# Performance work log

Hardware: AMD Instinct MI355X
Metric: run time of the kernel (lower is better)

The kernel has to match this reference:

```python
import jax, jax.numpy as jnp
import numpy as np
import math

B, L, D, H = 8, 2048, 1024, 1024


def setup_inputs() -> dict:
    key = jax.random.key(0)
    ks = jax.random.split(key, 6)
    scale = 1.0 / math.sqrt(D)
    return {
        "input_q": jax.random.normal(ks[0], (B, L, D), dtype=jnp.float32),
        "input_k": jax.random.normal(ks[1], (B, L, D), dtype=jnp.float32),
        "k_mask": jax.random.uniform(ks[2], (B, L), dtype=jnp.float32),
        "Wq": jax.random.normal(ks[3], (D, H), dtype=jnp.float32) * scale,
        "bq": jnp.zeros((H,), dtype=jnp.float32),
        "Wk": jax.random.normal(ks[4], (D, H), dtype=jnp.float32) * scale,
        "bk": jnp.zeros((H,), dtype=jnp.float32),
    }


def reference(input_q, input_k, k_mask, Wq, bq, Wk, bk):
    # Linear projections: (b, l, d) @ (d, h) -> (b, l, h)
    q = input_q @ Wq + bq
    k = input_k @ Wk + bk
    # Faithful to original: mask values become 0.0 or -1e9, then an
    # outer product bmm((b,l,1),(b,1,l)) builds the (b,l,l) additive mask.
    m = jnp.where(k_mask > 0.5, 0.0, -1000000000.0)  # (b, l)
    add_mask = m[:, :, None] * m[:, None, :]          # (b, l, l) outer product
    # Scaled dot-product scores
    attn = jnp.einsum("bqh,bkh->bqk", q, k) / math.sqrt(H)
    attn = jax.nn.softmax(attn + add_mask, axis=-1)
    # Weighted sum over the ORIGINAL input_k (not projected k), as in source
    out = jnp.einsum("bqk,bkd->bqd", attn, input_k)
    return out
```

## Files before the change

### kernel.cpp

```cpp
#include <hip/hip_runtime.h>

#define BATCH 8
#define SEQ   2048
#define DIM   1024

typedef __attribute__((ext_vector_type(8)))  short short8;
typedef __attribute__((ext_vector_type(4)))  short short4v;
typedef __attribute__((ext_vector_type(4)))  float floatx4;
typedef __attribute__((ext_vector_type(16))) float floatx16;

__device__ __forceinline__ unsigned short f32_to_bf16(float f) {
    union { float f; unsigned int u; } x; x.f = f;
    unsigned int r = x.u + 0x7fffu + ((x.u >> 16) & 1u);
    return (unsigned short)(r >> 16);
}

__device__ __forceinline__ float bf16_to_f32(unsigned short h) {
    union { unsigned int u; float f; } x; x.u = ((unsigned int)h) << 16;
    return x.f;
}

__device__ __forceinline__ void async_load16(const void* g, void* l) {
    __builtin_amdgcn_global_load_lds(
        (const __attribute__((address_space(1))) void*)g,
        (__attribute__((address_space(3))) void*)l, 16, 0, 0);
}

__global__ __launch_bounds__(256) void prep_misc(
    const float* __restrict__ mask, int* __restrict__ idx,
    int* __restrict__ cnt, int* __restrict__ padcnt, float* __restrict__ mavg,
    const float* __restrict__ Wq, unsigned short* __restrict__ Wqb,
    const float* __restrict__ Wk, unsigned short* __restrict__ Wkb,
    const float* __restrict__ bq, float* __restrict__ g0)
{
    __shared__ int wtot[4];
    __shared__ float rshared[4];
    const int id = blockIdx.x;
    const int t  = threadIdx.x;

    if (id < 8) {
        const int b = id;
        for (int d = t; d < DIM; d += 256) mavg[b * DIM + d] = 0.f;
        const float* mb = mask + b * SEQ;
        int flags[8]; int c = 0;
#pragma unroll
        for (int j = 0; j < 8; ++j) {
            flags[j] = (mb[t * 8 + j] > 0.5f) ? 1 : 0;
            c += flags[j];
        }
        int sc = c;
        for (int o = 1; o < 64; o <<= 1) {
            int v = __shfl_up(sc, o);
            if ((t & 63) >= o) sc += v;
        }
        const int lane = t & 63, wave = t >> 6;
        if (lane == 63) wtot[wave] = sc;
        __syncthreads();
        int woff = 0;
        for (int w = 0; w < wave; ++w) woff += wtot[w];
        int p = woff + sc - c;
#pragma unroll
        for (int j = 0; j < 8; ++j)
            if (flags[j]) idx[b * SEQ + (p++)] = t * 8 + j;
        __syncthreads();
        const int total = wtot[0] + wtot[1] + wtot[2] + wtot[3];
        if (t == 0) { cnt[b] = total; padcnt[b] = (total + 127) & ~127; }
        for (int q = total + t; q < SEQ; q += 256) idx[b * SEQ + q] = 0;
    } else if (id < 1032) {
        const int k = id - 8;
        const float* src = (k < 512) ? Wq : Wk;
        unsigned short* dst = (k < 512) ? Wqb : Wkb;
        const long i = ((long)(k & 511) * 256 + t) * 8;
        floatx4 v0 = *(const floatx4*)(src + i);
        floatx4 v1 = *(const floatx4*)(src + i + 4);
        short8 w;
#pragma unroll
        for (int j = 0; j < 4; ++j) w[j]     = (short)f32_to_bf16(v0[j]);
#pragma unroll
        for (int j = 0; j < 4; ++j) w[4 + j] = (short)f32_to_bf16(v1[j]);
        *(short8*)(dst + i) = w;
    } else {
        const int n = id - 1032;
        float s = 0.f;
        for (int h = t; h < DIM; h += 256) s += bq[h] * Wk[(long)n * DIM + h];
        for (int o = 32; o; o >>= 1) s += __shfl_xor(s, o);
        if ((t & 63) == 0) rshared[t >> 6] = s;
        __syncthreads();
        if (t == 0) g0[n] = rshared[0] + rshared[1] + rshared[2] + rshared[3];
    }
}

__global__ __launch_bounds__(256) void gather_cvt_q(
    const float* __restrict__ xq, const int* __restrict__ idx,
    const int* __restrict__ padcnt, unsigned short* __restrict__ qc)
{
    const int b = blockIdx.y;
    const int rc = blockIdx.x;
    if (rc >= padcnt[b]) return;
    const int src = idx[b * SEQ + rc];
    const float* s = xq + ((long)b * SEQ + src) * DIM + threadIdx.x * 4;
    unsigned short* d = qc + ((long)b * SEQ + rc) * DIM + threadIdx.x * 4;
    floatx4 v = *(const floatx4*)s;
    short4v w;
#pragma unroll
    for (int j = 0; j < 4; ++j) w[j] = (short)f32_to_bf16(v[j]);
    *(short4v*)d = w;
}

__global__ __launch_bounds__(256) void prep_kv(
    const float* __restrict__ xk, const float* __restrict__ mask,
    unsigned short* __restrict__ kbf, unsigned short* __restrict__ Vt,
    float* __restrict__ mavg)
{
    __shared__ float tile[64][65];
    __shared__ float msk[64];
    __shared__ float csum[4][64];
    const int b  = blockIdx.z;
    const int c0 = blockIdx.x * 64;
    const int r0 = blockIdx.y * 64;
    const int cg = threadIdx.x & 15;
    const int rr = threadIdx.x >> 4;
    const float* xb = xk + (long)b * SEQ * DIM;
    unsigned short* kb = kbf + (long)b * SEQ * DIM;
    unsigned short* vb = Vt + (long)b * DIM * SEQ;

    if (threadIdx.x < 64) msk[threadIdx.x] = mask[b * SEQ + r0 + threadIdx.x];

#pragma unroll
    for (int i = 0; i < 4; ++i) {
        const int row = rr + i * 16;
        const floatx4 v = *(const floatx4*)(xb + (long)(r0 + row) * DIM + c0 + cg * 4);
        short4v w;
#pragma unroll
        for (int j = 0; j < 4; ++j) {
            tile[row][cg * 4 + j] = v[j];
            w[j] = (short)f32_to_bf16(v[j]);
        }
        *(short4v*)(kb + (long)(r0 + row) * DIM + c0 + cg * 4) = w;
    }
    __syncthreads();

    {
        const int rgroup = threadIdx.x >> 6;
        const int c = threadIdx.x & 63;
        float s = 0.f;
#pragma unroll
        for (int r = 0; r < 16; ++r) {
            const int row = rgroup * 16 + r;
            s += (msk[row] <= 0.5f) ? tile[row][c] : 0.f;
        }
        csum[rgroup][c] = s;
    }

    {
        const int sg = threadIdx.x & 15;
        const int ch = threadIdx.x >> 4;
#pragma unroll
        for (int i = 0; i < 4; ++i) {
            const int c = ch + i * 16;
            short4v w;
#pragma unroll
            for (int j = 0; j < 4; ++j) w[j] = (short)f32_to_bf16(tile[sg * 4 + j][c]);
            *(short4v*)(vb + (long)(c0 + c) * SEQ + r0 + sg * 4) = w;
        }
    }
    __syncthreads();
    if (threadIdx.x < 64) {
        const int c = threadIdx.x;
        const float tot = csum[0][c] + csum[1][c] + csum[2][c] + csum[3][c];
        atomicAdd(&mavg[b * DIM + c0 + c], tot);
    }
}

template<bool C_BF16, bool BIAS, bool LIMIT, bool SCATTER, int FLAT, bool MFILL>
__global__ __launch_bounds__(256, 4) void gemm_bt(
    const unsigned short* __restrict__ A, const unsigned short* __restrict__ Bt,
    void* __restrict__ Cp, const float* __restrict__ bias,
    int N, int K, long sA, long sB, long sC, float scale,
    const int* __restrict__ mlim, const int* __restrict__ cntp,
    const int* __restrict__ idx, int sh,
    const float* __restrict__ kmask, const float* __restrict__ fmavg)
{
    if (MFILL && blockIdx.x >= 1024) {
        const int id2 = blockIdx.x - 1024;
        const int b = id2 >> 8;
        const int row = ((id2 & 255) << 3) + (threadIdx.x >> 5);
        if (kmask[b * SEQ + row] <= 0.5f) {
            const float inv = 1.0f / (float)(SEQ - cntp[b]);
            float* ob = (float*)Cp + ((long)b * SEQ + row) * DIM;
            const float* mv = fmavg + b * DIM;
            const int l32 = threadIdx.x & 31;
#pragma unroll
            for (int i = 0; i < 8; ++i) {
                const int d = (l32 + i * 32) * 4;
                const floatx4 s = *(const floatx4*)(mv + d);
                floatx4 o;
#pragma unroll
                for (int j = 0; j < 4; ++j) o[j] = s[j] * inv;
                *(floatx4*)(ob + d) = o;
            }
        }
        return;
    }

    int bx, by, bz;
    if (FLAT == 0) {
        bx = blockIdx.x; by = blockIdx.y; bz = blockIdx.z;
    } else {
        const int id = blockIdx.x;
        bz = id & 7;
        const int rem = id >> 3;
        const int m = (1 << sh) - 1;
        if (FLAT == 1) { bx = rem & m; by = rem >> sh; }
        else           { by = rem & m; bx = rem >> sh; }
    }
    const int row0 = bx * 128;
    if (LIMIT && row0 >= mlim[bz]) return;

    __shared__ unsigned short As[128 * 64];
    __shared__ unsigned short Bs[128 * 64];

    const int tid  = threadIdx.x;
    const int lane = tid & 63;
    const int wave = tid >> 6;
    const int wm   = wave >> 1;
    const int wn   = wave & 1;
    const int l31  = lane & 31;
    const int half = lane >> 5;
    const int x7   = lane & 7;
    const int col0 = by * 128;

    const int sr = lane >> 3;
    const int sq = ((lane & 7) ^ sr) * 8;

    const long K8 = (long)K * 8;
    const unsigned short* aRow =
        A + (long)bz * sA + (long)row0 * K + (long)(wave * 32 + sr) * K + sq;
    const unsigned short* bRow =
        Bt + (long)bz * sB + (long)col0 * K + (long)(wave * 32 + sr) * K + sq;

    floatx16 acc[2][2];
#pragma unroll
    for (int a = 0; a < 2; ++a)
#pragma unroll
        for (int b = 0; b < 2; ++b)
#pragma unroll
            for (int r = 0; r < 16; ++r) acc[a][b][r] = 0.f;

    const int raf[2] = { (wm * 64 +  0 + l31) * 64, (wm * 64 + 32 + l31) * 64 };
    const int rbf[2] = { (wn * 64 +  0 + l31) * 64, (wn * 64 + 32 + l31) * 64 };

    for (int kt = 0; kt < K; kt += 64) {
#pragma unroll
        for (int c = 0; c < 4; ++c) {
            const int chunk = wave * 4 + c;
            async_load16(aRow + kt + c * K8, As + chunk * 512);
            async_load16(bRow + kt + c * K8, Bs + chunk * 512);
        }
        __syncthreads();

#pragma unroll
        for (int ks = 0; ks < 4; ++ks) {
            const int sw = ((ks * 2 + half) ^ x7) << 3;
            short8 af[2], bf[2];
#pragma unroll
            for (int t = 0; t < 2; ++t) {
                af[t] = *(const short8*)(As + raf[t] + sw);
                bf[t] = *(const short8*)(Bs + rbf[t] + sw);
            }
#pragma unroll
            for (int tm = 0; tm < 2; ++tm)
#pragma unroll
                for (int tn = 0; tn < 2; ++tn)
                    acc[tm][tn] = __builtin_amdgcn_mfma_f32_32x32x16_bf16(
                        af[tm], bf[tn], acc[tm][tn], 0, 0, 0);
        }
        __syncthreads();
    }

    const long zC = (long)bz * sC;
    const int climit = SCATTER ? cntp[bz] : 0;
    const int* ridx  = SCATTER ? (idx + bz * SEQ) : (const int*)nullptr;
#pragma unroll
    for (int tn = 0; tn < 2; ++tn) {
        const int ccol = col0 + wn * 64 + tn * 32 + l31;
        float bv = 0.f;
        if (BIAS) bv = bias[ccol];
#pragma unroll
        for (int tm = 0; tm < 2; ++tm) {
            const int rbase = row0 + wm * 64 + tm * 32 + 4 * half;
#pragma unroll
            for (int r = 0; r < 16; ++r) {
                const int crow = rbase + (r & 3) + 8 * (r >> 2);
                float v = acc[tm][tn][r] * scale + bv;
                long orow = crow;
                if (SCATTER) {
                    if (crow >= climit) continue;
                    orow = ridx[crow];
                }
                const long ci = zC + orow * (long)N + ccol;
                if (C_BF16) ((unsigned short*)Cp)[ci] = f32_to_bf16(v);
                else        ((float*)Cp)[ci] = v;
            }
        }
    }
}

__global__ __launch_bounds__(256) void softmax_rows(
    unsigned short* __restrict__ S, const int* __restrict__ padcnt)
{
    const int b = blockIdx.x >> 11, rc = blockIdx.x & 2047;
    if (rc >= padcnt[b]) return;
    const long base = (long)blockIdx.x * SEQ + threadIdx.x * 8;
    const int lane = threadIdx.x & 63, wave = threadIdx.x >> 6;
    __shared__ float rbuf[8];

    short8 v = *(const short8*)(S + base);
    float x[8];
#pragma unroll
    for (int j = 0; j < 8; ++j) x[j] = bf16_to_f32((unsigned short)v[j]);

    float m = x[0];
#pragma unroll
    for (int j = 1; j < 8; ++j) m = fmaxf(m, x[j]);
    for (int o = 32; o; o >>= 1) m = fmaxf(m, __shfl_xor(m, o));
    if (lane == 0) rbuf[wave] = m;
    __syncthreads();
    m = fmaxf(fmaxf(rbuf[0], rbuf[1]), fmaxf(rbuf[2], rbuf[3]));

    float e[8], s = 0.f;
#pragma unroll
    for (int j = 0; j < 8; ++j) { e[j] = __expf(x[j] - m); s += e[j]; }
    for (int o = 32; o; o >>= 1) s += __shfl_xor(s, o);
    if (lane == 0) rbuf[4 + wave] = s;
    __syncthreads();
    s = rbuf[4] + rbuf[5] + rbuf[6] + rbuf[7];
    const float inv = 1.0f / s;

    short8 o8;
#pragma unroll
    for (int j = 0; j < 8; ++j) o8[j] = (short)f32_to_bf16(e[j] * inv);
    *(short8*)(S + base) = o8;
}

extern "C" void kernel_launch(void* const* d_in, const int* in_sizes, int n_in,
                              void* d_out, int out_size, void* d_ws, size_t ws_size,
                              hipStream_t stream) {
    (void)in_sizes; (void)n_in; (void)out_size;
    const float* input_q = (const float*)d_in[0];
    const float* input_k = (const float*)d_in[1];
    const float* k_mask  = (const float*)d_in[2];
    const float* Wq      = (const float*)d_in[3];
    const float* bq      = (const float*)d_in[4];
    const float* Wk      = (const float*)d_in[5];
    const float* bk      = (const float*)d_in[6];
    (void)bk;
    float* out = (float*)d_out;

    char* ws = (char*)d_ws;
    unsigned short* qc   = (unsigned short*)(ws);
    unsigned short* S    = (unsigned short*)(ws);
    unsigned short* qpp  = (unsigned short*)(ws + 67108864);
    unsigned short* Wqb  = (unsigned short*)(ws + 67108864);
    unsigned short* Wkb  = (unsigned short*)(ws + 69206016);
    unsigned short* kbf  = (unsigned short*)(ws + 100663296);
    unsigned short* Vt   = (unsigned short*)(ws + 134217728);
    unsigned short* Gt   = (unsigned short*)(ws + 167772160);
    float*          g0   = (float*)(ws + 169869312);
    float*          mavg = (float*)(ws + 169873408);
    int*            idx  = (int*)(ws + 169906176);
    int*            cnts = (int*)(ws + 169971712);
    int*            pcnt = (int*)(ws + 169971744);
    if (ws_size < 169971776) return;

    prep_misc<<<2056, 256, 0, stream>>>(k_mask, idx, cnts, pcnt, mavg,
                                        Wq, Wqb, Wk, Wkb, bq, g0);
    gather_cvt_q<<<dim3(SEQ, BATCH), 256, 0, stream>>>(input_q, idx, pcnt, qc);
    prep_kv<<<dim3(DIM / 64, SEQ / 64, BATCH), 256, 0, stream>>>(input_k, k_mask, kbf, Vt, mavg);

    gemm_bt<true, false, false, false, 0, false><<<dim3(8, 8, 1), 256, 0, stream>>>(
        Wkb, Wqb, Gt, nullptr, DIM, DIM, 0, 0, 0, 1.0f,
        nullptr, nullptr, nullptr, 0, nullptr, nullptr);

    gemm_bt<true, true, true, false, 2, false><<<8 * 16 * 8, 256, 0, stream>>>(
        qc, Gt, qpp, g0, DIM, DIM,
        (long)SEQ * DIM, 0, (long)SEQ * DIM, 1.0f,
        pcnt, nullptr, nullptr, 3, nullptr, nullptr);

    gemm_bt<true, false, true, false, 1, false><<<8 * 16 * 16, 256, 0, stream>>>(
        qpp, kbf, S, nullptr, SEQ, DIM,
        (long)SEQ * DIM, (long)SEQ * DIM, (long)SEQ * SEQ, 0.03125f,
        pcnt, nullptr, nullptr, 4, nullptr, nullptr);

    softmax_rows<<<BATCH * SEQ, 256, 0, stream>>>(S, pcnt);

    gemm_bt<false, false, true, true, 2, true><<<1024 + 2048, 256, 0, stream>>>(
        S, Vt, out, nullptr, DIM, SEQ,
        (long)SEQ * SEQ, (long)DIM * SEQ, (long)SEQ * DIM, 1.0f,
        pcnt, cnts, idx, 3, k_mask, mavg);
}
```

Before: 349.6 us.

## Fuse Wk·Wq GEMM, K/V prep and Q gather into one launch

Merges three independent launches (the small Gt weight GEMM, the K conversion/transpose/masked-sum kernel and the Q gather-convert kernel) into one kernel that dispatches on block id, with the GEMM body factored into a device function sharing one LDS buffer. The goal is to drop launch overhead and let the tiny 64-block GEMM overlap with the memory-bound prep work instead of running alone on a mostly idle GPU. The Q gather also changes from one block per row to one block per eight rows with 32 threads per row. The tradeoff is that every block reserves the GEMM-sized shared memory, which may lower occupancy for the prep blocks.

```diff
diff --git a/kernel.cpp b/kernel.cpp
--- a/kernel.cpp
+++ b/kernel.cpp
@@ -90,135 +90,18 @@
     }
 }
 
-__global__ __launch_bounds__(256) void gather_cvt_q(
-    const float* __restrict__ xq, const int* __restrict__ idx,
-    const int* __restrict__ padcnt, unsigned short* __restrict__ qc)
-{
-    const int b = blockIdx.y;
-    const int rc = blockIdx.x;
-    if (rc >= padcnt[b]) return;
-    const int src = idx[b * SEQ + rc];
-    const float* s = xq + ((long)b * SEQ + src) * DIM + threadIdx.x * 4;
-    unsigned short* d = qc + ((long)b * SEQ + rc) * DIM + threadIdx.x * 4;
-    floatx4 v = *(const floatx4*)s;
-    short4v w;
-#pragma unroll
-    for (int j = 0; j < 4; ++j) w[j] = (short)f32_to_bf16(v[j]);
-    *(short4v*)d = w;
-}
-
-__global__ __launch_bounds__(256) void prep_kv(
-    const float* __restrict__ xk, const float* __restrict__ mask,
-    unsigned short* __restrict__ kbf, unsigned short* __restrict__ Vt,
-    float* __restrict__ mavg)
-{
-    __shared__ float tile[64][65];
-    __shared__ float msk[64];
-    __shared__ float csum[4][64];
-    const int b  = blockIdx.z;
-    const int c0 = blockIdx.x * 64;
-    const int r0 = blockIdx.y * 64;
-    const int cg = threadIdx.x & 15;
-    const int rr = threadIdx.x >> 4;
-    const float* xb = xk + (long)b * SEQ * DIM;
-    unsigned short* kb = kbf + (long)b * SEQ * DIM;
-    unsigned short* vb = Vt + (long)b * DIM * SEQ;
-
-    if (threadIdx.x < 64) msk[threadIdx.x] = mask[b * SEQ + r0 + threadIdx.x];
-
-#pragma unroll
-    for (int i = 0; i < 4; ++i) {
-        const int row = rr + i * 16;
-        const floatx4 v = *(const floatx4*)(xb + (long)(r0 + row) * DIM + c0 + cg * 4);
-        short4v w;
-#pragma unroll
-        for (int j = 0; j < 4; ++j) {
-            tile[row][cg * 4 + j] = v[j];
-            w[j] = (short)f32_to_bf16(v[j]);
-        }
-        *(short4v*)(kb + (long)(r0 + row) * DIM + c0 + cg * 4) = w;
-    }
-    __syncthreads();
-
-    {
-        const int rgroup = threadIdx.x >> 6;
-        const int c = threadIdx.x & 63;
-        float s = 0.f;
-#pragma unroll
-        for (int r = 0; r < 16; ++r) {
-            const int row = rgroup * 16 + r;
-            s += (msk[row] <= 0.5f) ? tile[row][c] : 0.f;
-        }
-        csum[rgroup][c] = s;
-    }
-
-    {
-        const int sg = threadIdx.x & 15;
-        const int ch = threadIdx.x >> 4;
-#pragma unroll
-        for (int i = 0; i < 4; ++i) {
-            const int c = ch + i * 16;
-            short4v w;
-#pragma unroll
-            for (int j = 0; j < 4; ++j) w[j] = (short)f32_to_bf16(tile[sg * 4 + j][c]);
-            *(short4v*)(vb + (long)(c0 + c) * SEQ + r0 + sg * 4) = w;
-        }
-    }
-    __syncthreads();
-    if (threadIdx.x < 64) {
-        const int c = threadIdx.x;
-        const float tot = csum[0][c] + csum[1][c] + csum[2][c] + csum[3][c];
-        atomicAdd(&mavg[b * DIM + c0 + c], tot);
-    }
-}
-
-template<bool C_BF16, bool BIAS, bool LIMIT, bool SCATTER, int FLAT, bool MFILL>
-__global__ __launch_bounds__(256, 4) void gemm_bt(
+template<bool C_BF16, bool BIAS, bool LIMIT, bool SCATTER>
+__device__ __forceinline__ void gemm_tile_128(
+    unsigned short* __restrict__ As, unsigned short* __restrict__ Bs,
+    int bx, int by, int bz,
     const unsigned short* __restrict__ A, const unsigned short* __restrict__ Bt,
     void* __restrict__ Cp, const float* __restrict__ bias,
     int N, int K, long sA, long sB, long sC, float scale,
     const int* __restrict__ mlim, const int* __restrict__ cntp,
-    const int* __restrict__ idx, int sh,
-    const float* __restrict__ kmask, const float* __restrict__ fmavg)
+    const int* __restrict__ idx)
 {
-    if (MFILL && blockIdx.x >= 1024) {
-        const int id2 = blockIdx.x - 1024;
-        const int b = id2 >> 8;
-        const int row = ((id2 & 255) << 3) + (threadIdx.x >> 5);
-        if (kmask[b * SEQ + row] <= 0.5f) {
-            const float inv = 1.0f / (float)(SEQ - cntp[b]);
-            float* ob = (float*)Cp + ((long)b * SEQ + row) * DIM;
-            const float* mv = fmavg + b * DIM;
-            const int l32 = threadIdx.x & 31;
-#pragma unroll
-            for (int i = 0; i < 8; ++i) {
-                const int d = (l32 + i * 32) * 4;
-                const floatx4 s = *(const floatx4*)(mv + d);
-                floatx4 o;
-#pragma unroll
-                for (int j = 0; j < 4; ++j) o[j] = s[j] * inv;
-                *(floatx4*)(ob + d) = o;
-            }
-        }
-        return;
-    }
-
-    int bx, by, bz;
-    if (FLAT == 0) {
-        bx = blockIdx.x; by = blockIdx.y; bz = blockIdx.z;
-    } else {
-        const int id = blockIdx.x;
-        bz = id & 7;
-        const int rem = id >> 3;
-        const int m = (1 << sh) - 1;
-        if (FLAT == 1) { bx = rem & m; by = rem >> sh; }
-        else           { by = rem & m; bx = rem >> sh; }
-    }
     const int row0 = bx * 128;
     if (LIMIT && row0 >= mlim[bz]) return;
-
-    __shared__ unsigned short As[128 * 64];
-    __shared__ unsigned short Bs[128 * 64];
 
     const int tid  = threadIdx.x;
     const int lane = tid & 63;
@@ -301,6 +184,157 @@
                 const long ci = zC + orow * (long)N + ccol;
                 if (C_BF16) ((unsigned short*)Cp)[ci] = f32_to_bf16(v);
                 else        ((float*)Cp)[ci] = v;
+            }
+        }
+    }
+}
+
+template<bool C_BF16, bool BIAS, bool LIMIT, bool SCATTER, int FLAT, bool MFILL>
+__global__ __launch_bounds__(256, 4) void gemm_bt(
+    const unsigned short* __restrict__ A, const unsigned short* __restrict__ Bt,
+    void* __restrict__ Cp, const float* __restrict__ bias,
+    int N, int K, long sA, long sB, long sC, float scale,
+    const int* __restrict__ mlim, const int* __restrict__ cntp,
+    const int* __restrict__ idx, int sh,
+    const float* __restrict__ kmask, const float* __restrict__ fmavg)
+{
+    __shared__ unsigned short As[128 * 64];
+    __shared__ unsigned short Bs[128 * 64];
+
+    if (MFILL && blockIdx.x >= 1024) {
+        const int id2 = blockIdx.x - 1024;
+        const int b = id2 >> 8;
+        const int row = ((id2 & 255) << 3) + (threadIdx.x >> 5);
+        if (kmask[b * SEQ + row] <= 0.5f) {
+            const float inv = 1.0f / (float)(SEQ - cntp[b]);
+            float* ob = (float*)Cp + ((long)b * SEQ + row) * DIM;
+            const float* mv = fmavg + b * DIM;
+            const int l32 = threadIdx.x & 31;
+#pragma unroll
+            for (int i = 0; i < 8; ++i) {
+                const int d = (l32 + i * 32) * 4;
+                const floatx4 s = *(const floatx4*)(mv + d);
+                floatx4 o;
+#pragma unroll
+                for (int j = 0; j < 4; ++j) o[j] = s[j] * inv;
+                *(floatx4*)(ob + d) = o;
+            }
+        }
+        return;
+    }
+
+    int bx, by, bz;
+    if (FLAT == 0) {
+        bx = blockIdx.x; by = blockIdx.y; bz = blockIdx.z;
+    } else {
+        const int id = blockIdx.x;
+        bz = id & 7;
+        const int rem = id >> 3;
+        const int m = (1 << sh) - 1;
+        if (FLAT == 1) { bx = rem & m; by = rem >> sh; }
+        else           { by = rem & m; bx = rem >> sh; }
+    }
+    gemm_tile_128<C_BF16, BIAS, LIMIT, SCATTER>(
+        As, Bs, bx, by, bz, A, Bt, Cp, bias, N, K, sA, sB, sC, scale,
+        mlim, cntp, idx);
+}
+
+__global__ __launch_bounds__(256, 4) void fused_stage2(
+    const unsigned short* __restrict__ Wkb, const unsigned short* __restrict__ Wqb,
+    unsigned short* __restrict__ Gt,
+    const float* __restrict__ xq, const int* __restrict__ idx,
+    const int* __restrict__ padcnt, unsigned short* __restrict__ qc,
+    const float* __restrict__ xk, const float* __restrict__ mask,
+    unsigned short* __restrict__ kbf, unsigned short* __restrict__ Vt,
+    float* __restrict__ mavg)
+{
+    __shared__ unsigned short sbuf[2 * 128 * 64];
+    const int id = blockIdx.x;
+
+    if (id < 64) {
+        gemm_tile_128<true, false, false, false>(
+            sbuf, sbuf + 128 * 64, id & 7, id >> 3, 0,
+            Wkb, Wqb, Gt, nullptr, DIM, DIM, 0, 0, 0, 1.0f,
+            nullptr, nullptr, nullptr);
+    } else if (id < 64 + 4096) {
+        const int p  = id - 64;
+        const int c0 = (p & 15) * 64;
+        const int r0 = ((p >> 4) & 31) * 64;
+        const int b  = p >> 9;
+        float* tile = (float*)sbuf;
+        float* msk  = tile + 64 * 65;
+        float* csum = msk + 64;
+        const int cg = threadIdx.x & 15;
+        const int rr = threadIdx.x >> 4;
+        const float* xb = xk + (long)b * SEQ * DIM;
+        unsigned short* kb = kbf + (long)b * SEQ * DIM;
+        unsigned short* vb = Vt + (long)b * DIM * SEQ;
+
+        if (threadIdx.x < 64) msk[threadIdx.x] = mask[b * SEQ + r0 + threadIdx.x];
+
+#pragma unroll
+        for (int i = 0; i < 4; ++i) {
+            const int row = rr + i * 16;
+            const floatx4 v = *(const floatx4*)(xb + (long)(r0 + row) * DIM + c0 + cg * 4);
+            short4v w;
+#pragma unroll
+            for (int j = 0; j < 4; ++j) {
+                tile[row * 65 + cg * 4 + j] = v[j];
+                w[j] = (short)f32_to_bf16(v[j]);
+            }
+            *(short4v*)(kb + (long)(r0 + row) * DIM + c0 + cg * 4) = w;
+        }
+        __syncthreads();
+
+        {
+            const int rgroup = threadIdx.x >> 6;
+            const int c = threadIdx.x & 63;
+            float s = 0.f;
+#pragma unroll
+            for (int r = 0; r < 16; ++r) {
+                const int row = rgroup * 16 + r;
+                s += (msk[row] <= 0.5f) ? tile[row * 65 + c] : 0.f;
+            }
+            csum[rgroup * 64 + c] = s;
+        }
+
+        {
+            const int sg = threadIdx.x & 15;
+            const int ch = threadIdx.x >> 4;
+#pragma unroll
+            for (int i = 0; i < 4; ++i) {
+                const int c = ch + i * 16;
+                short4v w;
+#pragma unroll
+                for (int j = 0; j < 4; ++j)
+                    w[j] = (short)f32_to_bf16(tile[(sg * 4 + j) * 65 + c]);
+                *(short4v*)(vb + (long)(c0 + c) * SEQ + r0 + sg * 4) = w;
+            }
+        }
+        __syncthreads();
+        if (threadIdx.x < 64) {
+            const int c = threadIdx.x;
+            const float tot = csum[0 * 64 + c] + csum[1 * 64 + c] +
+                              csum[2 * 64 + c] + csum[3 * 64 + c];
+            atomicAdd(&mavg[b * DIM + c0 + c], tot);
+        }
+    } else {
+        const int g  = id - (64 + 4096);
+        const int b  = g >> 8;
+        const int rc = ((g & 255) << 3) + (threadIdx.x >> 5);
+        if (rc < padcnt[b]) {
+            const int src = idx[b * SEQ + rc];
+            const int l32 = threadIdx.x & 31;
+            const float* s = xq + ((long)b * SEQ + src) * DIM;
+            unsigned short* d = qc + ((long)b * SEQ + rc) * DIM;
+#pragma unroll
+            for (int i = 0; i < 8; ++i) {
+                const int c = (l32 + i * 32) * 4;
+                const floatx4 v = *(const floatx4*)(s + c);
+                short4v w;
+#pragma unroll
+                for (int j = 0; j < 4; ++j) w[j] = (short)f32_to_bf16(v[j]);
+                *(short4v*)(d + c) = w;
             }
         }
     }
@@ -375,12 +409,9 @@
 
     prep_misc<<<2056, 256, 0, stream>>>(k_mask, idx, cnts, pcnt, mavg,
                                         Wq, Wqb, Wk, Wkb, bq, g0);
-    gather_cvt_q<<<dim3(SEQ, BATCH), 256, 0, stream>>>(input_q, idx, pcnt, qc);
-    prep_kv<<<dim3(DIM / 64, SEQ / 64, BATCH), 256, 0, stream>>>(input_k, k_mask, kbf, Vt, mavg);
-
-    gemm_bt<true, false, false, false, 0, false><<<dim3(8, 8, 1), 256, 0, stream>>>(
-        Wkb, Wqb, Gt, nullptr, DIM, DIM, 0, 0, 0, 1.0f,
-        nullptr, nullptr, nullptr, 0, nullptr, nullptr);
+
+    fused_stage2<<<64 + 4096 + 2048, 256, 0, stream>>>(
+        Wkb, Wqb, Gt, input_q, idx, pcnt, qc, input_k, k_mask, kbf, Vt, mavg);
 
     gemm_bt<true, true, true, false, 2, false><<<8 * 16 * 8, 256, 0, stream>>>(
         qc, Gt, qpp, g0, DIM, DIM,
```

Result: faster. 324.7 us (-7.1%).
